# Performance work log

Hardware: AMD Instinct MI355X
Metric: run time of the kernel (lower is better)

The kernel has to match this reference:

```python
import jax, jax.numpy as jnp
import numpy as np

IN_FEATURES = 4096
OUT_FEATURES = 11008
GROUP_SIZE = 128
N_HIGH = 1024   # int(0.25*4096)//8*8
N_LOW = 3072    # (4096-1024)//8*8
M_TOKENS = 64


def unpack_6bit(packed, original_k):
    # packed: [K*3//4, N] uint8 values stored as int32
    _, N = packed.shape
    p = packed.reshape(original_k // 4, 3, N)
    b0, b1, b2 = p[:, 0], p[:, 1], p[:, 2]
    v0 = b0 & 63
    v1 = ((b0 >> 6) & 3) | ((b1 & 15) << 2)
    v2 = ((b1 >> 4) & 15) | ((b2 & 3) << 4)
    v3 = (b2 >> 2) & 63
    return jnp.stack([v0, v1, v2, v3], axis=1).reshape(original_k, N)


def unpack_5bit(packed, original_k):
    # packed: [K*5//8, N]
    _, N = packed.shape
    p = packed.reshape(original_k // 8, 5, N)
    b = [p[:, i] for i in range(5)]
    v0 = b[0] & 31
    v1 = ((b[0] >> 5) & 7) | ((b[1] & 3) << 3)
    v2 = (b[1] >> 2) & 31
    v3 = ((b[1] >> 7) & 1) | ((b[2] & 15) << 1)
    v4 = ((b[2] >> 4) & 15) | ((b[3] & 1) << 4)
    v5 = (b[3] >> 1) & 31
    v6 = ((b[3] >> 6) & 3) | ((b[4] & 7) << 2)
    v7 = (b[4] >> 3) & 31
    return jnp.stack([v0, v1, v2, v3, v4, v5, v6, v7], axis=1).reshape(original_k, N)


def dequant_region(W_q, scales, half_range):
    # W_q: [K, N] ints in [0, 2*half_range]; scales: [num_groups, N]
    K, N = W_q.shape
    G = scales.shape[0]
    Wg = (W_q.astype(jnp.float32) - float(half_range)).reshape(G, GROUP_SIZE, N)
    return (Wg * scales[:, None, :]).reshape(K, N)


def setup_inputs() -> dict:
    key = jax.random.key(0)
    ks = jax.random.split(key, 7)
    x = jax.random.normal(ks[0], (M_TOKENS, IN_FEATURES), dtype=jnp.float32)
    W_high_packed = jax.random.randint(ks[1], (N_HIGH * 3 // 4, OUT_FEATURES), 0, 256, dtype=jnp.int32)
    W_low_packed = jax.random.randint(ks[2], (N_LOW * 5 // 8, OUT_FEATURES), 0, 256, dtype=jnp.int32)
    scales_high = jax.random.uniform(ks[3], (N_HIGH // GROUP_SIZE, OUT_FEATURES), dtype=jnp.float32) * 0.02 + 1e-4
    scales_low = jax.random.uniform(ks[4], (N_LOW // GROUP_SIZE, OUT_FEATURES), dtype=jnp.float32) * 0.02 + 1e-4
    col_indices = jax.random.permutation(ks[5], IN_FEATURES).astype(jnp.int32)
    bias = jax.random.normal(ks[6], (OUT_FEATURES,), dtype=jnp.float32) * 0.02
    return {"x": x, "W_high_packed": W_high_packed, "W_low_packed": W_low_packed,
            "scales_high": scales_high, "scales_low": scales_low,
            "col_indices": col_indices, "bias": bias}


def reference(x, W_high_packed, W_low_packed, scales_high, scales_low, col_indices, bias):
    # Unpack mixed 6-bit / 5-bit weights and group-dequantize.
    Wq_high = unpack_6bit(W_high_packed, N_HIGH)          # [1024, N], 0..63
    Wq_low = unpack_5bit(W_low_packed, N_LOW)             # [3072, N], 0..31
    W_high = dequant_region(Wq_high, scales_high, 31)     # 6-bit half_range = 31
    W_low = dequant_region(Wq_low, scales_low, 15)        # 5-bit half_range = 15
    # Column-sensitivity reorder of activations, then split high/low regions.
    x_perm = x[:, col_indices]                            # [M, K]
    x_high = x_perm[:, :N_HIGH]
    x_low = x_perm[:, N_HIGH:N_HIGH + N_LOW]
    out = x_high @ W_high + x_low @ W_low + bias          # [M, N]
    return out
```

## Files before the change

### kernel.cpp

```cpp
#include <hip/hip_runtime.h>


#define NFEAT 11008
#define KTOT  4096

typedef _Float16 half8 __attribute__((ext_vector_type(8)));
typedef float    f32x4 __attribute__((ext_vector_type(4)));

__global__ __launch_bounds__(256) void prep_xfrag(const float* __restrict__ x,
                                                  const int* __restrict__ col,
                                                  _Float16* __restrict__ xfrag) {
    int idx = blockIdx.x * 256 + threadIdx.x;
    int j  = idx & 7;
    int l  = (idx >> 3) & 63;
    int mt = (idx >> 9) & 3;
    int s  = idx >> 11;
    int k  = s * 32 + ((l >> 4) << 3) + j;
    int m  = mt * 16 + (l & 15);
    xfrag[idx] = (_Float16)x[m * KTOT + col[k]];
}

__global__ __launch_bounds__(256) void gemm_kernel(const int* __restrict__ Wh,
                                                   const int* __restrict__ Wl,
                                                   const float* __restrict__ sh,
                                                   const float* __restrict__ sl,
                                                   const _Float16* __restrict__ xfrag,
                                                   float* __restrict__ dst,
                                                   int atomic_mode) {
    const int n0   = blockIdx.x * 64;
    const int kc   = blockIdx.y;
    const int tid  = threadIdx.x;
    const int lane = tid & 63;
    const int wave = tid >> 6;

    __shared__ _Float16 Wfrag[8 * 64 * 8 + 4 * 8];

    f32x4 acc[4];
#pragma unroll
    for (int i = 0; i < 4; ++i) acc[i] = (f32x4){0.f, 0.f, 0.f, 0.f};

    const int col  = lane;
    const int nt   = col >> 4;
    const int n_in = col & 15;

    for (int t = 0; t < 16; ++t) {
        if (kc == 0) {
            const float s = sh[(t >> 1) * NFEAT + n0 + col];
#pragma unroll
            for (int p = 0; p < 2; ++p) {
                const int kg2 = p * 4 + wave;
                const int k   = t * 64 + kg2 * 8;
                const int G   = k >> 2;
                const int* bp = Wh + (3 * G) * NFEAT + n0 + col;
                int b0 = bp[0],         b1 = bp[NFEAT],     b2 = bp[2 * NFEAT];
                int b3 = bp[3 * NFEAT], b4 = bp[4 * NFEAT], b5 = bp[5 * NFEAT];
                int v[8];
                v[0] = b0 & 63;
                v[1] = ((b0 >> 6) & 3) | ((b1 & 15) << 2);
                v[2] = ((b1 >> 4) & 15) | ((b2 & 3) << 4);
                v[3] = (b2 >> 2) & 63;
                v[4] = b3 & 63;
                v[5] = ((b3 >> 6) & 3) | ((b4 & 15) << 2);
                v[6] = ((b4 >> 4) & 15) | ((b5 & 3) << 4);
                v[7] = (b5 >> 2) & 63;
                half8 w;
#pragma unroll
                for (int j = 0; j < 8; ++j) w[j] = (_Float16)(((float)v[j] - 31.0f) * s);
                const int q = kg2 >> 2, quad = kg2 & 3;
                const int off = (((nt * 2 + q) * 64 + quad * 16 + n_in) + nt) * 8;
                *(half8*)&Wfrag[off] = w;
            }
        } else {
            const int kl0 = (kc - 1) * 1024 + t * 64;
            const float s = sl[(kl0 >> 7) * NFEAT + n0 + col];
#pragma unroll
            for (int p = 0; p < 2; ++p) {
                const int kg8 = p * 4 + wave;
                const int kl  = kl0 + kg8 * 8;
                const int G   = kl >> 3;
                const int* bp = Wl + (5 * G) * NFEAT + n0 + col;
                int b0 = bp[0], b1 = bp[NFEAT], b2 = bp[2 * NFEAT];
                int b3 = bp[3 * NFEAT], b4 = bp[4 * NFEAT];
                int v[8];
                v[0] = b0 & 31;
                v[1] = ((b0 >> 5) & 7) | ((b1 & 3) << 3);
                v[2] = (b1 >> 2) & 31;
                v[3] = ((b1 >> 7) & 1) | ((b2 & 15) << 1);
                v[4] = ((b2 >> 4) & 15) | ((b3 & 1) << 4);
                v[5] = (b3 >> 1) & 31;
                v[6] = ((b3 >> 6) & 3) | ((b4 & 7) << 2);
                v[7] = (b4 >> 3) & 31;
                half8 w;
#pragma unroll
                for (int j = 0; j < 8; ++j) w[j] = (_Float16)(((float)v[j] - 15.0f) * s);
                const int q = kg8 >> 2, quad = kg8 & 3;
                const int off = (((nt * 2 + q) * 64 + quad * 16 + n_in) + nt) * 8;
                *(half8*)&Wfrag[off] = w;
            }
        }
        __syncthreads();

#pragma unroll
        for (int q = 0; q < 2; ++q) {
            const int sg = kc * 32 + t * 2 + q;
            half8 a = *(const half8*)(xfrag + (((sg * 4 + wave) * 64 + lane) << 3));
#pragma unroll
            for (int j = 0; j < 4; ++j) {
                half8 b = *(half8*)&Wfrag[(((j * 2 + q) * 64 + lane) + j) * 8];
                acc[j] = __builtin_amdgcn_mfma_f32_16x16x32_f16(a, b, acc[j], 0, 0, 0);
            }
        }
        __syncthreads();
    }

    const int rb = wave * 16 + ((lane >> 4) << 2);
    const int cb = lane & 15;
    if (atomic_mode) {
#pragma unroll
        for (int j = 0; j < 4; ++j)
#pragma unroll
            for (int r = 0; r < 4; ++r)
                atomicAdd(&dst[(rb + r) * NFEAT + n0 + j * 16 + cb], acc[j][r]);
    } else {
        float* base = dst + (size_t)kc * 64 * NFEAT;
#pragma unroll
        for (int j = 0; j < 4; ++j)
#pragma unroll
            for (int r = 0; r < 4; ++r)
                base[(rb + r) * NFEAT + n0 + j * 16 + cb] = acc[j][r];
    }
}

__global__ __launch_bounds__(256) void reduce_out(const float* __restrict__ part,
                                                  const float* __restrict__ bias,
                                                  float* __restrict__ out) {
    const int idx = blockIdx.x * 256 + threadIdx.x;
    const int f   = idx * 4;
    const int n   = f % NFEAT;
    f32x4 a = *(const f32x4*)(part + f);
    f32x4 b = *(const f32x4*)(part + 704512 + f);
    f32x4 c = *(const f32x4*)(part + 2 * 704512 + f);
    f32x4 d = *(const f32x4*)(part + 3 * 704512 + f);
    f32x4 bi = *(const f32x4*)(bias + n);
    *(f32x4*)(out + f) = a + b + c + d + bi;
}

__global__ __launch_bounds__(256) void init_bias(const float* __restrict__ bias,
                                                 float* __restrict__ out) {
    const int idx = blockIdx.x * 256 + threadIdx.x;
    out[idx] = bias[idx % NFEAT];
}

extern "C" void kernel_launch(void* const* d_in, const int* in_sizes, int n_in,
                              void* d_out, int out_size, void* d_ws, size_t ws_size,
                              hipStream_t stream) {
    const float* x    = (const float*)d_in[0];
    const int*   Wh   = (const int*)d_in[1];
    const int*   Wl   = (const int*)d_in[2];
    const float* sh   = (const float*)d_in[3];
    const float* sl   = (const float*)d_in[4];
    const int*   col  = (const int*)d_in[5];
    const float* bias = (const float*)d_in[6];
    float* out = (float*)d_out;

    _Float16* xfrag = (_Float16*)d_ws;
    const size_t xfrag_bytes = 64 * KTOT * sizeof(_Float16);
    const size_t part_bytes  = 4ull * 64 * NFEAT * sizeof(float);

    prep_xfrag<<<1024, 256, 0, stream>>>(x, col, xfrag);

    dim3 grid(172, 4);
    if (ws_size >= xfrag_bytes + part_bytes) {
        float* part = (float*)((char*)d_ws + xfrag_bytes);
        gemm_kernel<<<grid, 256, 0, stream>>>(Wh, Wl, sh, sl, xfrag, part, 0);
        reduce_out<<<688, 256, 0, stream>>>(part, bias, out);
    } else {
        init_bias<<<2752, 256, 0, stream>>>(bias, out);
        gemm_kernel<<<grid, 256, 0, stream>>>(Wh, Wl, sh, sl, xfrag, out, 1);
    }
}
```

Measured before the change: 176.5 us.

## Rewrite quantized GEMM with split high/low kernels, double-buffered LDS, and fast fp16 dequant

Splits the GEMM into separate templated kernels for the 6-bit and 5-bit regions and splits K across 8 partitions instead of 4. Each thread now loads vectorized int4 weight words, and the next tile's global loads are issued while MFMAs run on a double-buffered LDS tile. Dequantization uses the 0x6400 magic-number trick with packed half2 arithmetic, and prep_xfrag writes half8 vectors. The aim is to cut serialized load latency and dequant ALU cost. The costs are more partial-sum traffic in the reduction, an extra launch, and rounding the scale to fp16 before multiplying.

Measured after the change: 185.5 us. 1.05x slower.

```diff
diff --git a/kernel.cpp b/kernel.cpp
--- a/kernel.cpp
+++ b/kernel.cpp
@@ -5,112 +5,142 @@
 #define KTOT  4096
 
 typedef _Float16 half8 __attribute__((ext_vector_type(8)));
+typedef _Float16 half2 __attribute__((ext_vector_type(2)));
 typedef float    f32x4 __attribute__((ext_vector_type(4)));
+typedef int      i32x4 __attribute__((ext_vector_type(4)));
+
+union H8 { half8 v; half2 h[4]; _Float16 e[8]; };
+
+__device__ __forceinline__ half2 dq2(int a, int b, half2 off, half2 s) {
+    unsigned u = 0x64006400u | (unsigned)a | ((unsigned)b << 16);
+    half2 h = __builtin_bit_cast(half2, u);
+    return (h - off) * s;
+}
 
 __global__ __launch_bounds__(256) void prep_xfrag(const float* __restrict__ x,
                                                   const int* __restrict__ col,
                                                   _Float16* __restrict__ xfrag) {
-    int idx = blockIdx.x * 256 + threadIdx.x;
-    int j  = idx & 7;
-    int l  = (idx >> 3) & 63;
-    int mt = (idx >> 9) & 3;
-    int s  = idx >> 11;
-    int k  = s * 32 + ((l >> 4) << 3) + j;
+    int u  = blockIdx.x * 256 + threadIdx.x;
+    int l  = u & 63;
+    int mt = (u >> 6) & 3;
+    int s  = u >> 8;
     int m  = mt * 16 + (l & 15);
-    xfrag[idx] = (_Float16)x[m * KTOT + col[k]];
-}
-
-__global__ __launch_bounds__(256) void gemm_kernel(const int* __restrict__ Wh,
-                                                   const int* __restrict__ Wl,
-                                                   const float* __restrict__ sh,
-                                                   const float* __restrict__ sl,
-                                                   const _Float16* __restrict__ xfrag,
-                                                   float* __restrict__ dst,
-                                                   int atomic_mode) {
+    int kb = s * 32 + ((l >> 4) << 3);
+    H8 w;
+#pragma unroll
+    for (int j = 0; j < 8; ++j)
+        w.e[j] = (_Float16)x[m * KTOT + col[kb + j]];
+    *(half8*)(xfrag + (size_t)u * 8) = w.v;
+}
+
+template <bool HIGH>
+__global__ __launch_bounds__(256, 4) void gemm_kernel(const int* __restrict__ W,
+                                                      const float* __restrict__ S,
+                                                      const _Float16* __restrict__ xfrag,
+                                                      float* __restrict__ dst,
+                                                      int titers, int sg_off,
+                                                      int atomic_mode) {
     const int n0   = blockIdx.x * 64;
-    const int kc   = blockIdx.y;
     const int tid  = threadIdx.x;
     const int lane = tid & 63;
     const int wave = tid >> 6;
-
-    __shared__ _Float16 Wfrag[8 * 64 * 8 + 4 * 8];
+    const int cg   = tid & 15;
+    const int kg   = tid >> 4;
+    const int kgl  = kg & 3;
+    const int colb = n0 + cg * 4;
+    const int kbase = blockIdx.y * titers * 128;
+
+    __shared__ _Float16 lds[2 * 8192];
+    const int wchunk0 = ((cg >> 2) * 4 + (kg >> 2)) * 64 + kgl * 16 + (cg & 3) * 4;
+    const int laneX   = lane ^ (lane >> 4);
 
     f32x4 acc[4];
 #pragma unroll
     for (int i = 0; i < 4; ++i) acc[i] = (f32x4){0.f, 0.f, 0.f, 0.f};
 
-    const int col  = lane;
-    const int nt   = col >> 4;
-    const int n_in = col & 15;
-
-    for (int t = 0; t < 16; ++t) {
-        if (kc == 0) {
-            const float s = sh[(t >> 1) * NFEAT + n0 + col];
-#pragma unroll
-            for (int p = 0; p < 2; ++p) {
-                const int kg2 = p * 4 + wave;
-                const int k   = t * 64 + kg2 * 8;
-                const int G   = k >> 2;
-                const int* bp = Wh + (3 * G) * NFEAT + n0 + col;
-                int b0 = bp[0],         b1 = bp[NFEAT],     b2 = bp[2 * NFEAT];
-                int b3 = bp[3 * NFEAT], b4 = bp[4 * NFEAT], b5 = bp[5 * NFEAT];
-                int v[8];
-                v[0] = b0 & 63;
-                v[1] = ((b0 >> 6) & 3) | ((b1 & 15) << 2);
-                v[2] = ((b1 >> 4) & 15) | ((b2 & 3) << 4);
-                v[3] = (b2 >> 2) & 63;
-                v[4] = b3 & 63;
-                v[5] = ((b3 >> 6) & 3) | ((b4 & 15) << 2);
-                v[6] = ((b4 >> 4) & 15) | ((b5 & 3) << 4);
-                v[7] = (b5 >> 2) & 63;
-                half8 w;
-#pragma unroll
-                for (int j = 0; j < 8; ++j) w[j] = (_Float16)(((float)v[j] - 31.0f) * s);
-                const int q = kg2 >> 2, quad = kg2 & 3;
-                const int off = (((nt * 2 + q) * 64 + quad * 16 + n_in) + nt) * 8;
-                *(half8*)&Wfrag[off] = w;
+    i32x4 R[6];
+    f32x4 s4;
+
+    auto load_tile = [&](int t) {
+        const int kb = kbase + t * 128;
+        if constexpr (HIGH) {
+            const int* p = W + (size_t)((kb >> 2) * 3 + kg * 6) * NFEAT + colb;
+#pragma unroll
+            for (int r = 0; r < 6; ++r) R[r] = *(const i32x4*)(p + (size_t)r * NFEAT);
+        } else {
+            const int* p = W + (size_t)((kb >> 3) * 5 + kg * 5) * NFEAT + colb;
+#pragma unroll
+            for (int r = 0; r < 5; ++r) R[r] = *(const i32x4*)(p + (size_t)r * NFEAT);
+        }
+        s4 = *(const f32x4*)(S + (size_t)(kb >> 7) * NFEAT + colb);
+    };
+
+    auto dq_store = [&](int buf) {
+        _Float16* base = lds + (buf << 13);
+        const _Float16 offv = HIGH ? (_Float16)1055.0f : (_Float16)1039.0f;
+        const half2 off = {offv, offv};
+#pragma unroll
+        for (int cc = 0; cc < 4; ++cc) {
+            int v0, v1, v2, v3, v4, v5, v6, v7;
+            if constexpr (HIGH) {
+                int b0 = R[0][cc], b1 = R[1][cc], b2 = R[2][cc],
+                    b3 = R[3][cc], b4 = R[4][cc], b5 = R[5][cc];
+                v0 = b0 & 63;
+                v1 = ((b0 >> 6) & 3) | ((b1 & 15) << 2);
+                v2 = ((b1 >> 4) & 15) | ((b2 & 3) << 4);
+                v3 = (b2 >> 2) & 63;
+                v4 = b3 & 63;
+                v5 = ((b3 >> 6) & 3) | ((b4 & 15) << 2);
+                v6 = ((b4 >> 4) & 15) | ((b5 & 3) << 4);
+                v7 = (b5 >> 2) & 63;
+            } else {
+                int b0 = R[0][cc], b1 = R[1][cc], b2 = R[2][cc],
+                    b3 = R[3][cc], b4 = R[4][cc];
+                v0 = b0 & 31;
+                v1 = ((b0 >> 5) & 7) | ((b1 & 3) << 3);
+                v2 = (b1 >> 2) & 31;
+                v3 = ((b1 >> 7) & 1) | ((b2 & 15) << 1);
+                v4 = ((b2 >> 4) & 15) | ((b3 & 1) << 4);
+                v5 = (b3 >> 1) & 31;
+                v6 = ((b3 >> 6) & 3) | ((b4 & 7) << 2);
+                v7 = (b4 >> 3) & 31;
             }
-        } else {
-            const int kl0 = (kc - 1) * 1024 + t * 64;
-            const float s = sl[(kl0 >> 7) * NFEAT + n0 + col];
-#pragma unroll
-            for (int p = 0; p < 2; ++p) {
-                const int kg8 = p * 4 + wave;
-                const int kl  = kl0 + kg8 * 8;
-                const int G   = kl >> 3;
-                const int* bp = Wl + (5 * G) * NFEAT + n0 + col;
-                int b0 = bp[0], b1 = bp[NFEAT], b2 = bp[2 * NFEAT];
-                int b3 = bp[3 * NFEAT], b4 = bp[4 * NFEAT];
-                int v[8];
-                v[0] = b0 & 31;
-                v[1] = ((b0 >> 5) & 7) | ((b1 & 3) << 3);
-                v[2] = (b1 >> 2) & 31;
-                v[3] = ((b1 >> 7) & 1) | ((b2 & 15) << 1);
-                v[4] = ((b2 >> 4) & 15) | ((b3 & 1) << 4);
-                v[5] = (b3 >> 1) & 31;
-                v[6] = ((b3 >> 6) & 3) | ((b4 & 7) << 2);
-                v[7] = (b4 >> 3) & 31;
-                half8 w;
-#pragma unroll
-                for (int j = 0; j < 8; ++j) w[j] = (_Float16)(((float)v[j] - 15.0f) * s);
-                const int q = kg8 >> 2, quad = kg8 & 3;
-                const int off = (((nt * 2 + q) * 64 + quad * 16 + n_in) + nt) * 8;
-                *(half8*)&Wfrag[off] = w;
+            _Float16 sc = (_Float16)s4[cc];
+            half2 s2 = {sc, sc};
+            H8 w;
+            w.h[0] = dq2(v0, v1, off, s2);
+            w.h[1] = dq2(v2, v3, off, s2);
+            w.h[2] = dq2(v4, v5, off, s2);
+            w.h[3] = dq2(v6, v7, off, s2);
+            *(half8*)(base + (size_t)(wchunk0 + (cc ^ kgl)) * 8) = w.v;
+        }
+    };
+
+    auto do_mfma = [&](int buf, int t) {
+        const _Float16* Bb = lds + (buf << 13);
+        const int sg = sg_off + (kbase >> 5) + t * 4;
+        half8 a[4];
+#pragma unroll
+        for (int q = 0; q < 4; ++q)
+            a[q] = *(const half8*)(xfrag + (size_t)(((sg + q) * 4 + wave) * 64 + lane) * 8);
+#pragma unroll
+        for (int q = 0; q < 4; ++q) {
+#pragma unroll
+            for (int nt = 0; nt < 4; ++nt) {
+                half8 b = *(const half8*)(Bb + (size_t)((nt * 4 + q) * 64 + laneX) * 8);
+                acc[nt] = __builtin_amdgcn_mfma_f32_16x16x32_f16(a[q], b, acc[nt], 0, 0, 0);
             }
         }
+    };
+
+    load_tile(0);
+    int buf = 0;
+    for (int t = 0; t < titers; ++t) {
+        dq_store(buf);
         __syncthreads();
-
-#pragma unroll
-        for (int q = 0; q < 2; ++q) {
-            const int sg = kc * 32 + t * 2 + q;
-            half8 a = *(const half8*)(xfrag + (((sg * 4 + wave) * 64 + lane) << 3));
-#pragma unroll
-            for (int j = 0; j < 4; ++j) {
-                half8 b = *(half8*)&Wfrag[(((j * 2 + q) * 64 + lane) + j) * 8];
-                acc[j] = __builtin_amdgcn_mfma_f32_16x16x32_f16(a, b, acc[j], 0, 0, 0);
-            }
-        }
-        __syncthreads();
+        if (t + 1 < titers) load_tile(t + 1);
+        do_mfma(buf, t);
+        buf ^= 1;
     }
 
     const int rb = wave * 16 + ((lane >> 4) << 2);
@@ -120,29 +150,27 @@
         for (int j = 0; j < 4; ++j)
 #pragma unroll
             for (int r = 0; r < 4; ++r)
-                atomicAdd(&dst[(rb + r) * NFEAT + n0 + j * 16 + cb], acc[j][r]);
+                atomicAdd(&dst[(size_t)(rb + r) * NFEAT + n0 + j * 16 + cb], acc[j][r]);
     } else {
-        float* base = dst + (size_t)kc * 64 * NFEAT;
+        float* o = dst + (size_t)blockIdx.y * 64 * NFEAT;
 #pragma unroll
         for (int j = 0; j < 4; ++j)
 #pragma unroll
             for (int r = 0; r < 4; ++r)
-                base[(rb + r) * NFEAT + n0 + j * 16 + cb] = acc[j][r];
+                o[(size_t)(rb + r) * NFEAT + n0 + j * 16 + cb] = acc[j][r];
     }
 }
 
 __global__ __launch_bounds__(256) void reduce_out(const float* __restrict__ part,
                                                   const float* __restrict__ bias,
-                                                  float* __restrict__ out) {
+                                                  float* __restrict__ out, int P) {
     const int idx = blockIdx.x * 256 + threadIdx.x;
     const int f   = idx * 4;
     const int n   = f % NFEAT;
-    f32x4 a = *(const f32x4*)(part + f);
-    f32x4 b = *(const f32x4*)(part + 704512 + f);
-    f32x4 c = *(const f32x4*)(part + 2 * 704512 + f);
-    f32x4 d = *(const f32x4*)(part + 3 * 704512 + f);
-    f32x4 bi = *(const f32x4*)(bias + n);
-    *(f32x4*)(out + f) = a + b + c + d + bi;
+    f32x4 s = *(const f32x4*)(bias + n);
+    for (int p = 0; p < P; ++p)
+        s += *(const f32x4*)(part + (size_t)p * 704512 + f);
+    *(f32x4*)(out + f) = s;
 }
 
 __global__ __launch_bounds__(256) void init_bias(const float* __restrict__ bias,
@@ -164,18 +192,26 @@
     float* out = (float*)d_out;
 
     _Float16* xfrag = (_Float16*)d_ws;
-    const size_t xfrag_bytes = 64 * KTOT * sizeof(_Float16);
-    const size_t part_bytes  = 4ull * 64 * NFEAT * sizeof(float);
-
-    prep_xfrag<<<1024, 256, 0, stream>>>(x, col, xfrag);
-
-    dim3 grid(172, 4);
-    if (ws_size >= xfrag_bytes + part_bytes) {
-        float* part = (float*)((char*)d_ws + xfrag_bytes);
-        gemm_kernel<<<grid, 256, 0, stream>>>(Wh, Wl, sh, sl, xfrag, part, 0);
-        reduce_out<<<688, 256, 0, stream>>>(part, bias, out);
+    const size_t xb      = (size_t)64 * KTOT * sizeof(_Float16);
+    const size_t pstride = (size_t)64 * NFEAT;
+
+    prep_xfrag<<<128, 256, 0, stream>>>(x, col, xfrag);
+
+    if (ws_size >= xb + 8 * pstride * sizeof(float)) {
+        float* part = (float*)((char*)d_ws + xb);
+        gemm_kernel<true><<<dim3(172, 2), 256, 0, stream>>>(Wh, sh, xfrag, part, 4, 0, 0);
+        gemm_kernel<false><<<dim3(172, 6), 256, 0, stream>>>(Wl, sl, xfrag,
+                                                             part + 2 * pstride, 4, 32, 0);
+        reduce_out<<<688, 256, 0, stream>>>(part, bias, out, 8);
+    } else if (ws_size >= xb + 4 * pstride * sizeof(float)) {
+        float* part = (float*)((char*)d_ws + xb);
+        gemm_kernel<true><<<dim3(172, 1), 256, 0, stream>>>(Wh, sh, xfrag, part, 8, 0, 0);
+        gemm_kernel<false><<<dim3(172, 3), 256, 0, stream>>>(Wl, sl, xfrag,
+                                                             part + pstride, 8, 32, 0);
+        reduce_out<<<688, 256, 0, stream>>>(part, bias, out, 4);
     } else {
         init_bias<<<2752, 256, 0, stream>>>(bias, out);
-        gemm_kernel<<<grid, 256, 0, stream>>>(Wh, Wl, sh, sl, xfrag, out, 1);
+        gemm_kernel<true><<<dim3(172, 2), 256, 0, stream>>>(Wh, sh, xfrag, out, 4, 0, 1);
+        gemm_kernel<false><<<dim3(172, 6), 256, 0, stream>>>(Wl, sl, xfrag, out, 4, 32, 1);
     }
 }
```
